# Kernel tuning notes

Hardware: AMD Instinct MI355X
Metric: run time of the kernel (lower is better)

The kernel has to match this reference:

```python
import jax, jax.numpy as jnp
import numpy as np

VOCAB, P, K, B, L, R = 50257, 512, 64, 32, 2048, 5


def setup_inputs() -> dict:
    key = jax.random.key(0)
    k1, k2, k3, k4, k5, k6, k7 = jax.random.split(key, 7)
    return {
        "x": jax.random.randint(k1, (B, L), 0, VOCAB, dtype=jnp.int32),
        "V": jax.random.normal(k2, (VOCAB, P), dtype=jnp.float32),
        "C": jax.random.normal(k3, (K, P), dtype=jnp.float32),
        "f1_w": jax.random.normal(k4, (2 * R + 1,), dtype=jnp.float32),
        "f1_b": jax.random.normal(k5, (K,), dtype=jnp.float32),
        "f2_w": jax.random.normal(k6, (K, P), dtype=jnp.float32),
        "f2_b": jax.random.normal(k7, (K,), dtype=jnp.float32),
    }


def reference(x, V, C, f1_w, f1_b, f2_w, f2_b):
    b, l = x.shape
    k, p = C.shape
    w = f1_w.shape[0]
    r = (w - 1) // 2
    emb = V[x]                                              # [B,L,P] embedding lookup
    x_hat = emb / jnp.linalg.norm(emb, axis=2, keepdims=True)
    l_hat = C / jnp.linalg.norm(C, axis=1, keepdims=True)
    G = jnp.einsum('kp,blp->bkl', l_hat, x_hat)             # cosine sim [B,K,L]
    # sliding-window dot product == depthwise 1D cross-correlation, 'same' padding
    u = jax.lax.conv_general_dilated(
        G.reshape(b * k, 1, l), f1_w.reshape(1, 1, w),
        window_strides=(1,), padding=[(r, r)],
        dimension_numbers=('NCH', 'OIH', 'NCH'),
    ).reshape(b, k, l)
    m = jax.nn.relu(u + f1_b[None, :, None])                # [B,K,L]
    beta = jax.nn.softmax(m.max(axis=1), axis=1)            # max over labels, softmax over seq -> [B,L]
    pooled = jnp.mean(beta[:, :, None] * emb, axis=1)       # [B,P]
    return pooled @ f2_w.T + f2_b                           # [B,K]
```

## Files before the change

kernel.cpp:

```cpp
#include <hip/hip_runtime.h>
#include <hip/hip_bf16.h>

#define PP     512
#define KK     64
#define BB     32
#define LLEN   2048
#define NPOS   (BB * LLEN)

typedef __attribute__((ext_vector_type(8)))  short short8;
typedef __attribute__((ext_vector_type(16))) float float16;

__device__ inline unsigned int pack_bf2(float lo, float hi) {
    __hip_bfloat162 h = __float22bfloat162_rn(make_float2(lo, hi));
    unsigned int u;
    __builtin_memcpy(&u, &h, 4);
    return u;
}
__device__ inline float bf_lo(unsigned int v) { return __uint_as_float(v << 16); }
__device__ inline float bf_hi(unsigned int v) { return __uint_as_float(v & 0xffff0000u); }

__global__ void k1_prep(const float* __restrict__ C, const float* __restrict__ f2w,
                        ushort* __restrict__ Bu) {
    const int n = blockIdx.x;
    const float* src = (n < 64) ? (C + n * PP) : (f2w + (n - 64) * PP);
    const int t = threadIdx.x;
    float v0 = src[t];
    float v1 = src[t + 256];
    __shared__ float red[256];
    red[t] = v0 * v0 + v1 * v1;
    __syncthreads();
    for (int s = 128; s > 0; s >>= 1) {
        if (t < s) red[t] += red[t + s];
        __syncthreads();
    }
    const float inv = (n < 64) ? rsqrtf(red[0]) : 1.f;
    Bu[(((t >> 3)       * 128 + n) << 3) + (t & 7)] = (ushort)(pack_bf2(v0 * inv, 0.f) & 0xffffu);
    Bu[((((t + 256) >> 3)) * 128 + n) * 8 + (t & 7)] = (ushort)(pack_bf2(v1 * inv, 0.f) & 0xffffu);
}

__launch_bounds__(256)
__global__ void k2_gemm(const int* __restrict__ x, const float* __restrict__ V,
                        const uint4* __restrict__ Bu4,
                        unsigned int* __restrict__ Gt2, unsigned int* __restrict__ E2p) {
    __shared__ uint4 sA[64 * 16];
    __shared__ int   stok[64];
    __shared__ float rnorm[64];

    const int tid  = threadIdx.x;
    const int lane = tid & 63;
    const int wv   = tid >> 6;
    const int f    = tid & 15;
    const int mrow = tid >> 4;

    if (tid < 64) stok[tid] = x[blockIdx.x * 64 + tid];
    __syncthreads();

    float16 acc0, acc1;
#pragma unroll
    for (int i = 0; i < 16; ++i) { acc0[i] = 0.f; acc1[i] = 0.f; }
    float nacc[4];
#pragma unroll
    for (int i = 0; i < 4; ++i) nacc[i] = 0.f;

    const int mt = (wv & 1) * 32;
    const int nh = (wv >> 1) * 64;

    float4 pa[4][2];
#pragma unroll
    for (int i = 0; i < 4; ++i) {
        const float* src = V + (size_t)stok[mrow + i * 16] * PP + f * 8;
        pa[i][0] = ((const float4*)src)[0];
        pa[i][1] = ((const float4*)src)[1];
    }

    for (int kc = 0; kc < 4; ++kc) {
        __syncthreads();
#pragma unroll
        for (int i = 0; i < 4; ++i) {
            const int m = mrow + i * 16;
            const float4 a = pa[i][0];
            const float4 b = pa[i][1];
            uint4 wq;
            wq.x = pack_bf2(a.x, a.y); wq.y = pack_bf2(a.z, a.w);
            wq.z = pack_bf2(b.x, b.y); wq.w = pack_bf2(b.z, b.w);
            sA[m * 16 + (f ^ (m & 7))] = wq;
            float s2 = 0.f;
            s2 = fmaf(a.x, a.x, s2); s2 = fmaf(a.y, a.y, s2);
            s2 = fmaf(a.z, a.z, s2); s2 = fmaf(a.w, a.w, s2);
            s2 = fmaf(b.x, b.x, s2); s2 = fmaf(b.y, b.y, s2);
            s2 = fmaf(b.z, b.z, s2); s2 = fmaf(b.w, b.w, s2);
            nacc[i] += s2;
        }
        if (kc < 3) {
#pragma unroll
            for (int i = 0; i < 4; ++i) {
                const float* src = V + (size_t)stok[mrow + i * 16] * PP + (kc + 1) * 128 + f * 8;
                pa[i][0] = ((const float4*)src)[0];
                pa[i][1] = ((const float4*)src)[1];
            }
        } else {
#pragma unroll
            for (int i = 0; i < 4; ++i) {
                float r = nacc[i];
                r += __shfl_down(r, 8, 16);
                r += __shfl_down(r, 4, 16);
                r += __shfl_down(r, 2, 16);
                r += __shfl_down(r, 1, 16);
                if (f == 0) rnorm[mrow + i * 16] = rsqrtf(r);
            }
        }
        __syncthreads();

#pragma unroll
        for (int kb = 0; kb < 8; ++kb) {
            const int ff = kb * 2 + (lane >> 5);
            const int mq = mt + (lane & 31);
            const uint4 av = sA[mq * 16 + (ff ^ (mq & 7))];
            const uint4 b0 = Bu4[(kc * 16 + ff) * 128 + nh + (lane & 31)];
            const uint4 b1 = Bu4[(kc * 16 + ff) * 128 + nh + 32 + (lane & 31)];
            short8 a8, t0, t1;
            __builtin_memcpy(&a8, &av, 16);
            __builtin_memcpy(&t0, &b0, 16);
            __builtin_memcpy(&t1, &b1, 16);
            acc0 = __builtin_amdgcn_mfma_f32_32x32x16_bf16(a8, t0, acc0, 0, 0, 0);
            acc1 = __builtin_amdgcn_mfma_f32_32x32x16_bf16(a8, t1, acc1, 0, 0, 0);
        }
    }

    const size_t posBase = (size_t)blockIdx.x * 64;
#pragma unroll
    for (int reg = 0; reg < 16; ++reg) {
        const int r  = (reg & 3) + 8 * (reg >> 2) + 4 * (lane >> 5);
        const int mq = mt + r;
        const size_t p = posBase + mq;
        if (wv < 2) {
            const float rn = rnorm[mq];
            Gt2[p * 32 + (lane & 31)] = pack_bf2(acc0[reg] * rn, acc1[reg] * rn);
        } else {
            E2p[p * 32 + (lane & 31)] = pack_bf2(acc0[reg], acc1[reg]);
        }
    }
}

__global__ void k3_convpool(const unsigned int* __restrict__ Gt2,
                            const unsigned int* __restrict__ E2p,
                            const float* __restrict__ f1w, const float* __restrict__ f1b,
                            float* __restrict__ pool) {
    __shared__ unsigned int sT[74 * 33];
    __shared__ float smv[64];
    __shared__ float sp[64];
    __shared__ float sscal[2];
    __shared__ float sred[8][64];

    const int b  = blockIdx.x >> 5;
    const int l0 = (blockIdx.x & 31) * 64;
    const int t  = threadIdx.x;

    for (int idx = t; idx < 74 * 32; idx += 256) {
        const int row = idx >> 5, col = idx & 31;
        const int gl = l0 - 5 + row;
        sT[row * 33 + col] = (gl >= 0 && gl < LLEN)
            ? Gt2[((size_t)b * LLEN + gl) * 32 + col] : 0u;
    }
    __syncthreads();

    float w[11];
#pragma unroll
    for (int j = 0; j < 11; ++j) w[j] = f1w[j];
    const int j = t & 31;
    const int h = t >> 5;
    const float bias0 = f1b[j], bias1 = f1b[j + 32];
#pragma unroll
    for (int i = 0; i < 8; ++i) {
        const int lr = i * 8 + h;
        float u0 = 0.f, u1 = 0.f;
#pragma unroll
        for (int tap = 0; tap < 11; ++tap) {
            const unsigned int v = sT[(lr + tap) * 33 + j];
            u0 = fmaf(bf_lo(v), w[tap], u0);
            u1 = fmaf(bf_hi(v), w[tap], u1);
        }
        float m = fmaxf(fmaxf(u0 + bias0, 0.f), fmaxf(u1 + bias1, 0.f));
#pragma unroll
        for (int off = 16; off > 0; off >>= 1)
            m = fmaxf(m, __shfl_xor(m, off, 64));
        if (j == 0) smv[lr] = m;
    }
    __syncthreads();

    if (t < 64) {
        float v = smv[t];
#pragma unroll
        for (int off = 32; off > 0; off >>= 1)
            v = fmaxf(v, __shfl_xor(v, off, 64));
        if (t == 0) sscal[0] = v;
    }
    __syncthreads();
    const float mx = sscal[0];
    if (t < 64) sp[t] = __expf(smv[t] - mx);
    __syncthreads();
    if (t < 64) {
        float s = sp[t];
#pragma unroll
        for (int off = 32; off > 0; off >>= 1)
            s += __shfl_xor(s, off, 64);
        if (t == 0) sscal[1] = s;
    }

    float a0 = 0.f, a1 = 0.f;
#pragma unroll
    for (int i = 0; i < 8; ++i) {
        const int l = i * 8 + h;
        const float wgt = sp[l];
        const unsigned int e = E2p[((size_t)b * LLEN + l0 + l) * 32 + j];
        a0 = fmaf(wgt, bf_lo(e), a0);
        a1 = fmaf(wgt, bf_hi(e), a1);
    }
    sred[h][j]      = a0;
    sred[h][j + 32] = a1;
    __syncthreads();
    if (t < 64) {
        float r = 0.f;
#pragma unroll
        for (int hh = 0; hh < 8; ++hh) r += sred[hh][t];
        float* dst = pool + (size_t)blockIdx.x * 68;
        dst[t] = r;
        if (t == 0) { dst[64] = sscal[0]; dst[65] = sscal[1]; }
    }
}

__global__ void k6_final(const float* __restrict__ pool, const float* __restrict__ f2b,
                         float* __restrict__ out) {
    const int b = blockIdx.x;
    const int k = threadIdx.x;
    float M = -1e30f;
#pragma unroll
    for (int c = 0; c < 32; ++c)
        M = fmaxf(M, pool[(size_t)(b * 32 + c) * 68 + 64]);
    float tot = 0.f, num = 0.f;
#pragma unroll
    for (int c = 0; c < 32; ++c) {
        const float* pc = pool + (size_t)(b * 32 + c) * 68;
        const float sc = __expf(pc[64] - M);
        tot = fmaf(sc, pc[65], tot);
        num = fmaf(sc, pc[k], num);
    }
    out[b * KK + k] = (num / tot) * (1.f / 2048.f) + f2b[k];
}

extern "C" void kernel_launch(void* const* d_in, const int* in_sizes, int n_in,
                              void* d_out, int out_size, void* d_ws, size_t ws_size,
                              hipStream_t stream) {
    const int*   x   = (const int*)d_in[0];
    const float* V   = (const float*)d_in[1];
    const float* C   = (const float*)d_in[2];
    const float* f1w = (const float*)d_in[3];
    const float* f1b = (const float*)d_in[4];
    const float* f2w = (const float*)d_in[5];
    const float* f2b = (const float*)d_in[6];
    float* out = (float*)d_out;

    float* ws = (float*)d_ws;
    ushort* Bu = (ushort*)ws;
    unsigned int* Gt2 = (unsigned int*)(ws + 32768);
    unsigned int* E2p = Gt2 + (size_t)NPOS * 32;
    float* pool = (float*)(E2p + (size_t)NPOS * 32);

    k1_prep    <<<128, 256, 0, stream>>>(C, f2w, Bu);
    k2_gemm    <<<NPOS / 64, 256, 0, stream>>>(x, V, (const uint4*)Bu, Gt2, E2p);
    k3_convpool<<<BB * 32, 256, 0, stream>>>(Gt2, E2p, f1w, f1b, pool);
    k6_final   <<<BB, 64, 0, stream>>>(pool, f2b, out);
}
```

Baseline: 198.8 us.

## Stage full embedding rows in LDS with all gathers issued upfront

The GEMM kernel now issues every global load for a block's 64 embedding rows at once (4 threads per row, 32 float4 each), converts them to bf16 into a 64KB LDS tile covering the whole P dimension, then runs one uninterrupted MFMA loop over the 32 k-steps. This replaces the four-stage chunked loop, which had register double-buffering and two barriers per chunk. The goal is more memory-level parallelism on the random row gather and fewer synchronisations. In exchange, LDS use grows to 64KB per block and each thread holds 32 float4 in registers, which may cut occupancy.

```diff
diff --git a/kernel.cpp b/kernel.cpp
--- a/kernel.cpp
+++ b/kernel.cpp
@@ -42,102 +42,89 @@
 __global__ void k2_gemm(const int* __restrict__ x, const float* __restrict__ V,
                         const uint4* __restrict__ Bu4,
                         unsigned int* __restrict__ Gt2, unsigned int* __restrict__ E2p) {
-    __shared__ uint4 sA[64 * 16];
+    __shared__ uint4 sA[64 * 64];
     __shared__ int   stok[64];
     __shared__ float rnorm[64];
 
     const int tid  = threadIdx.x;
     const int lane = tid & 63;
     const int wv   = tid >> 6;
-    const int f    = tid & 15;
-    const int mrow = tid >> 4;
+    const int r    = tid >> 2;
+    const int q    = tid & 3;
 
     if (tid < 64) stok[tid] = x[blockIdx.x * 64 + tid];
     __syncthreads();
 
+    const float* src = V + (size_t)stok[r] * PP + q * 4;
+    const int swzr = r & 7;
+    float nrm = 0.f;
+
+    float4 pa[16];
+#pragma unroll
+    for (int g = 0; g < 16; ++g) pa[g] = ((const float4*)src)[g * 4];
+    float4 pb[16];
+#pragma unroll
+    for (int g = 0; g < 16; ++g) pb[g] = ((const float4*)src)[(g + 16) * 4];
+
+#pragma unroll
+    for (int g = 0; g < 16; ++g) {
+        const float4 a = pa[g];
+        nrm = fmaf(a.x, a.x, fmaf(a.y, a.y, fmaf(a.z, a.z, fmaf(a.w, a.w, nrm))));
+        uint2 w2; w2.x = pack_bf2(a.x, a.y); w2.y = pack_bf2(a.z, a.w);
+        const int f = g * 2 + (q >> 1);
+        ((uint2*)&sA[r * 64 + (f ^ swzr)])[q & 1] = w2;
+    }
+#pragma unroll
+    for (int g = 0; g < 16; ++g) {
+        const float4 a = pb[g];
+        nrm = fmaf(a.x, a.x, fmaf(a.y, a.y, fmaf(a.z, a.z, fmaf(a.w, a.w, nrm))));
+        uint2 w2; w2.x = pack_bf2(a.x, a.y); w2.y = pack_bf2(a.z, a.w);
+        const int f = (g + 16) * 2 + (q >> 1);
+        ((uint2*)&sA[r * 64 + (f ^ swzr)])[q & 1] = w2;
+    }
+
+    nrm += __shfl_xor(nrm, 1, 64);
+    nrm += __shfl_xor(nrm, 2, 64);
+    if (q == 0) rnorm[r] = rsqrtf(nrm);
+    __syncthreads();
+
     float16 acc0, acc1;
 #pragma unroll
     for (int i = 0; i < 16; ++i) { acc0[i] = 0.f; acc1[i] = 0.f; }
-    float nacc[4];
-#pragma unroll
-    for (int i = 0; i < 4; ++i) nacc[i] = 0.f;
-
-    const int mt = (wv & 1) * 32;
-    const int nh = (wv >> 1) * 64;
-
-    float4 pa[4][2];
-#pragma unroll
-    for (int i = 0; i < 4; ++i) {
-        const float* src = V + (size_t)stok[mrow + i * 16] * PP + f * 8;
-        pa[i][0] = ((const float4*)src)[0];
-        pa[i][1] = ((const float4*)src)[1];
-    }
-
-    for (int kc = 0; kc < 4; ++kc) {
-        __syncthreads();
-#pragma unroll
-        for (int i = 0; i < 4; ++i) {
-            const int m = mrow + i * 16;
-            const float4 a = pa[i][0];
-            const float4 b = pa[i][1];
-            uint4 wq;
-            wq.x = pack_bf2(a.x, a.y); wq.y = pack_bf2(a.z, a.w);
-            wq.z = pack_bf2(b.x, b.y); wq.w = pack_bf2(b.z, b.w);
-            sA[m * 16 + (f ^ (m & 7))] = wq;
-            float s2 = 0.f;
-            s2 = fmaf(a.x, a.x, s2); s2 = fmaf(a.y, a.y, s2);
-            s2 = fmaf(a.z, a.z, s2); s2 = fmaf(a.w, a.w, s2);
-            s2 = fmaf(b.x, b.x, s2); s2 = fmaf(b.y, b.y, s2);
-            s2 = fmaf(b.z, b.z, s2); s2 = fmaf(b.w, b.w, s2);
-            nacc[i] += s2;
-        }
-        if (kc < 3) {
-#pragma unroll
-            for (int i = 0; i < 4; ++i) {
-                const float* src = V + (size_t)stok[mrow + i * 16] * PP + (kc + 1) * 128 + f * 8;
-                pa[i][0] = ((const float4*)src)[0];
-                pa[i][1] = ((const float4*)src)[1];
-            }
+
+    const int mt  = (wv & 1) * 32;
+    const int nh  = (wv >> 1) * 64;
+    const int l31 = lane & 31;
+    const int cc  = lane >> 5;
+    const int mq  = mt + l31;
+    const int abase = mq * 64;
+    const int aswz  = mq & 7;
+
+#pragma unroll 8
+    for (int ks = 0; ks < 32; ++ks) {
+        const int ff = ks * 2 + cc;
+        const uint4 av = sA[abase + (ff ^ aswz)];
+        const uint4 b0 = Bu4[ff * 128 + nh + l31];
+        const uint4 b1 = Bu4[ff * 128 + nh + 32 + l31];
+        short8 a8, t0, t1;
+        __builtin_memcpy(&a8, &av, 16);
+        __builtin_memcpy(&t0, &b0, 16);
+        __builtin_memcpy(&t1, &b1, 16);
+        acc0 = __builtin_amdgcn_mfma_f32_32x32x16_bf16(a8, t0, acc0, 0, 0, 0);
+        acc1 = __builtin_amdgcn_mfma_f32_32x32x16_bf16(a8, t1, acc1, 0, 0, 0);
+    }
+
+    const size_t posBase = (size_t)blockIdx.x * 64;
+#pragma unroll
+    for (int reg = 0; reg < 16; ++reg) {
+        const int rr = (reg & 3) + 8 * (reg >> 2) + 4 * (lane >> 5);
+        const int m  = mt + rr;
+        const size_t p = posBase + m;
+        if (wv < 2) {
+            const float rn = rnorm[m];
+            Gt2[p * 32 + l31] = pack_bf2(acc0[reg] * rn, acc1[reg] * rn);
         } else {
-#pragma unroll
-            for (int i = 0; i < 4; ++i) {
-                float r = nacc[i];
-                r += __shfl_down(r, 8, 16);
-                r += __shfl_down(r, 4, 16);
-                r += __shfl_down(r, 2, 16);
-                r += __shfl_down(r, 1, 16);
-                if (f == 0) rnorm[mrow + i * 16] = rsqrtf(r);
-            }
-        }
-        __syncthreads();
-
-#pragma unroll
-        for (int kb = 0; kb < 8; ++kb) {
-            const int ff = kb * 2 + (lane >> 5);
-            const int mq = mt + (lane & 31);
-            const uint4 av = sA[mq * 16 + (ff ^ (mq & 7))];
-            const uint4 b0 = Bu4[(kc * 16 + ff) * 128 + nh + (lane & 31)];
-            const uint4 b1 = Bu4[(kc * 16 + ff) * 128 + nh + 32 + (lane & 31)];
-            short8 a8, t0, t1;
-            __builtin_memcpy(&a8, &av, 16);
-            __builtin_memcpy(&t0, &b0, 16);
-            __builtin_memcpy(&t1, &b1, 16);
-            acc0 = __builtin_amdgcn_mfma_f32_32x32x16_bf16(a8, t0, acc0, 0, 0, 0);
-            acc1 = __builtin_amdgcn_mfma_f32_32x32x16_bf16(a8, t1, acc1, 0, 0, 0);
-        }
-    }
-
-    const size_t posBase = (size_t)blockIdx.x * 64;
-#pragma unroll
-    for (int reg = 0; reg < 16; ++reg) {
-        const int r  = (reg & 3) + 8 * (reg >> 2) + 4 * (lane >> 5);
-        const int mq = mt + r;
-        const size_t p = posBase + mq;
-        if (wv < 2) {
-            const float rn = rnorm[mq];
-            Gt2[p * 32 + (lane & 31)] = pack_bf2(acc0[reg] * rn, acc1[reg] * rn);
-        } else {
-            E2p[p * 32 + (lane & 31)] = pack_bf2(acc0[reg], acc1[reg]);
+            E2p[p * 32 + l31] = pack_bf2(acc0[reg], acc1[reg]);
         }
     }
 }
```

Result: faster. 190.3 us (-4.3%).
